# Kernel optimization log

Hardware: AMD Instinct MI355X
Metric: run time of the kernel (lower is better)

The kernel has to match this reference:

```python
import jax, jax.numpy as jnp
import numpy as np

B, N1, N2, D, L, H = 2, 384, 384, 128, 3, 128
DM_MIN = 0.5


def _gat_layer(x, adj, W, Wb, A, gW, gb):
    # GAT_gate from jaechanglim/DTI_PDBbind: attention softmax over dim 1, gated residual
    h = x @ W + Wb                                   # [B,N,D]
    e = jnp.einsum('bjl,bkl->bjk', h @ A, h)
    e = e + jnp.swapaxes(e, 1, 2)
    att = jnp.where(adj > 0, e, -9e15)
    att = jax.nn.softmax(att, axis=1) * adj
    h_prime = jax.nn.relu(jnp.einsum('bij,bjk->bik', att, h))
    coeff = jax.nn.sigmoid(jnp.concatenate([x, h_prime], -1) @ gW + gb)  # [B,N,1]
    return coeff * x + (1.0 - coeff) * h_prime


def _pair_mlp(h1g, h2g, W1, b1, W2, b2):
    # MLP(concat(h1_i, h2_j)) without materializing the [B,N1,N2,2D] concat:
    # split W1 into ligand / protein halves and broadcast-add the projections.
    p1 = jnp.einsum('bnd,dk->bnk', h1g, W1[:D])      # [B,N1,H]
    p2 = jnp.einsum('bmd,dk->bmk', h2g, W1[D:])      # [B,N2,H]
    hid = jax.nn.relu(p1[:, :, None, :] + p2[:, None, :, :] + b1)  # [B,N1,N2,H]
    return (hid @ W2 + b2)[..., 0]                   # [B,N1,N2]


def reference(h1, adj1, h2, dmv, charge1, charge2, vdw_epsilon, vdw_sigma,
              delta_uff, valid1, valid2, no_metal1, no_metal2,
              node_W, gat_W, gat_Wb, gat_A, gat_gW, gat_gb,
              pair_W1, pair_b1, pair_W2, pair_b2,
              vdw_coeff, duff_coeff, int_W1, int_b1, int_W2, int_b2):
    h1g = h1 @ node_W
    h2g = h2 @ node_W
    for i in range(L):  # only ligand graph is convolved (as in the source)
        h1g = _gat_layer(h1g, adj1, gat_W[i], gat_Wb[i], gat_A[i], gat_gW[i], gat_gb[i])

    dm = jnp.sqrt(jnp.sum(dmv * dmv, -1) + 1e-10)    # [B,N1,N2]
    dm = jnp.where(dm < DM_MIN, 1e10, dm)

    # coulomb term (pair MLPs 0,1)
    cA = jax.nn.sigmoid(_pair_mlp(h1g, h2g, pair_W1[0], pair_b1[0], pair_W2[0], pair_b2[0]))
    cN = jax.nn.sigmoid(_pair_mlp(h1g, h2g, pair_W1[1], pair_b1[1], pair_W2[1], pair_b2[1])) * 2.0 + 1.0
    charge12 = charge1[:, :, None] * charge2[:, None, :]
    e_c = cA * charge12 * jnp.power(1.0 / dm, cN)
    e_c = e_c * valid1[:, :, None] * valid2[:, None, :]
    e_c = jnp.clip(e_c, -100.0, 100.0)
    e_c = jnp.sum(e_c, axis=(1, 2))[:, None]

    # vdw term (pair MLPs 2=A sigmoid, 3=B tanh, 4=N sigmoid)
    vA = (jax.nn.sigmoid(_pair_mlp(h1g, h2g, pair_W1[2], pair_b1[2], pair_W2[2], pair_b2[2])) * 0.6 + 0.7)
    vA = vA * (vdw_coeff[0] * vdw_coeff[0]) * vdw_epsilon
    vB = jnp.tanh(_pair_mlp(h1g, h2g, pair_W1[3], pair_b1[3], pair_W2[3], pair_b2[3])) * 0.6 + 0.7
    vN = jax.nn.sigmoid(_pair_mlp(h1g, h2g, pair_W1[4], pair_b1[4], pair_W2[4], pair_b2[4])) * 2.0 + 5.0
    dm0 = vdw_sigma * vB
    dm0 = jnp.where(dm0 < 1e-4, 1.0, dm0)
    r = jnp.power(dm0 / dm, vN)
    e_v = vA * (r * r - 2.0 * r)                     # (dm0/dm)^(2N) - 2(dm0/dm)^N
    e_v = e_v * no_metal1[:, :, None] * no_metal2[:, None, :]
    e_v = jnp.minimum(e_v, 100.0)
    e_v = jnp.sum(e_v, axis=(1, 2))[:, None]

    # conformational energy difference term
    e_u = (duff_coeff[0] * duff_coeff[0] * delta_uff)[:, None]

    # learned intercept from pooled ligand features
    hs = jnp.sum(h1g * valid1[..., None], axis=1)
    inter = jax.nn.relu(hs @ int_W1 + int_b1) @ int_W2 + int_b2

    return jnp.concatenate([e_c, e_v, e_u, inter], -1)  # [B,4]


def setup_inputs() -> dict:
    key = jax.random.key(0)
    ks = jax.random.split(key, 24)
    inp = {}
    inp['h1'] = jax.random.normal(ks[0], (B, N1, 54), jnp.float32)
    inp['h2'] = jax.random.normal(ks[1], (B, N2, 54), jnp.float32)
    a = jax.random.uniform(ks[2], (B, N1, N1))
    adj = (a > 0.9).astype(jnp.float32)
    adj = jnp.maximum(adj, jnp.swapaxes(adj, 1, 2))
    inp['adj1'] = jnp.maximum(adj, jnp.eye(N1, dtype=jnp.float32)[None])
    inp['dmv'] = jax.random.normal(ks[3], (B, N1, N2, 3), jnp.float32) * 3.0
    inp['charge1'] = jax.random.normal(ks[4], (B, N1), jnp.float32) * 0.3
    inp['charge2'] = jax.random.normal(ks[5], (B, N2), jnp.float32) * 0.3
    inp['vdw_epsilon'] = jax.random.uniform(ks[6], (B, N1, N2), jnp.float32) * 0.3
    inp['vdw_sigma'] = 3.0 + jax.random.uniform(ks[7], (B, N1, N2), jnp.float32)
    inp['delta_uff'] = jax.random.uniform(ks[8], (B,), jnp.float32) * 5.0
    inp['valid1'] = jnp.ones((B, N1), jnp.float32)
    inp['valid2'] = jnp.ones((B, N2), jnp.float32)
    inp['no_metal1'] = jnp.ones((B, N1), jnp.float32)
    inp['no_metal2'] = jnp.ones((B, N2), jnp.float32)
    # parameters
    inp['node_W'] = jax.random.normal(ks[9], (54, D), jnp.float32) * 0.1
    inp['gat_W'] = jax.random.normal(ks[10], (L, D, D), jnp.float32) * (1.0 / np.sqrt(D))
    inp['gat_Wb'] = jnp.zeros((L, D), jnp.float32)
    inp['gat_A'] = jax.random.normal(ks[11], (L, D, D), jnp.float32) * 0.05
    inp['gat_gW'] = jax.random.normal(ks[12], (L, 2 * D, 1), jnp.float32) * 0.05
    inp['gat_gb'] = jnp.zeros((L, 1), jnp.float32)
    inp['pair_W1'] = jax.random.normal(ks[13], (5, 2 * D, H), jnp.float32) * 0.05
    inp['pair_b1'] = jnp.zeros((5, H), jnp.float32)
    inp['pair_W2'] = jax.random.normal(ks[14], (5, H, 1), jnp.float32) * 0.1
    inp['pair_b2'] = jnp.zeros((5, 1), jnp.float32)
    inp['vdw_coeff'] = jnp.array([0.02], jnp.float32)
    inp['duff_coeff'] = jnp.array([0.1], jnp.float32)
    inp['int_W1'] = jax.random.normal(ks[15], (D, H), jnp.float32) * 0.05
    inp['int_b1'] = jnp.zeros((H,), jnp.float32)
    inp['int_W2'] = jax.random.normal(ks[16], (H, 1), jnp.float32) * 0.1
    inp['int_b2'] = jnp.zeros((1,), jnp.float32)
    return inp
```

## Files before the change

### kernel.cpp

```cpp
#include <hip/hip_runtime.h>
#include <math.h>

#define NN 384
#define DD 128
#define HH 128

__device__ __forceinline__ float sigmoidf_(float x) { return 1.f / (1.f + __expf(-x)); }
__device__ __forceinline__ float tanhf_(float x)    { return 1.f - 2.f / (__expf(2.f * x) + 1.f); }

__global__ __launch_bounds__(256) void k_start(
    const float* __restrict__ h1, const float* __restrict__ h2,
    const float* __restrict__ nW,
    const float* __restrict__ W, const float* __restrict__ Wb, const float* __restrict__ A,
    const float* __restrict__ pW1,
    const float* __restrict__ delta_uff, const float* __restrict__ duff,
    float* __restrict__ h1g, float* __restrict__ h2g,
    float* __restrict__ hb, float* __restrict__ hAb,
    float* __restrict__ hT, float* __restrict__ hAT,
    float* __restrict__ p2q, float* __restrict__ out) {
  int blk = blockIdx.x, tid = threadIdx.x, c = tid & 127, g = tid >> 7;
  if (blk == 0 && tid < 8) {
    int bb = tid >> 2, cc = tid & 3;
    out[tid] = (cc == 2) ? duff[0] * duff[0] * delta_uff[bb] : 0.f;
  }
  if (blk < 384) {
    int r = blk * 2 + g;
    const float* xr = h1 + r * 54;
    float acc = 0.f;
#pragma unroll 6
    for (int k = 0; k < 54; ++k) acc += xr[k] * nW[k * DD + c];
    h1g[r * DD + c] = acc;
    __syncthreads();
    const float4* xr4 = (const float4*)(h1g + r * DD);
    float a0 = 0.f, a1 = 0.f;
#pragma unroll 4
    for (int k4 = 0; k4 < DD / 4; ++k4) {
      float4 xv = xr4[k4]; int k = 4 * k4;
      a0 += xv.x * W[k * DD + c] + xv.z * W[(k + 2) * DD + c];
      a1 += xv.y * W[(k + 1) * DD + c] + xv.w * W[(k + 3) * DD + c];
    }
    float hv = a0 + a1 + Wb[c];
    hb[r * DD + c] = hv; hT[c * 768 + r] = hv;
    __syncthreads();
    const float4* hr4 = (const float4*)(hb + r * DD);
    a0 = 0.f; a1 = 0.f;
#pragma unroll 4
    for (int k4 = 0; k4 < DD / 4; ++k4) {
      float4 xv = hr4[k4]; int k = 4 * k4;
      a0 += xv.x * A[k * DD + c] + xv.z * A[(k + 2) * DD + c];
      a1 += xv.y * A[(k + 1) * DD + c] + xv.w * A[(k + 3) * DD + c];
    }
    float av = a0 + a1;
    hAb[r * DD + c] = av; hAT[c * 768 + r] = av;
  } else {
    int r0 = (blk - 384) * 2;
    int r = r0 + g;
    const float* xr = h2 + r * 54;
    float acc = 0.f;
#pragma unroll 6
    for (int k = 0; k < 54; ++k) acc += xr[k] * nW[k * DD + c];
    h2g[r * DD + c] = acc;
    __syncthreads();
    const float* xbase = h2g + r0 * DD;
    for (int o = tid; o < 640; o += 256) {
      int m = o >> 7, hc = o & 127;
      const float* Wcol = pW1 + (m * 256 + 128) * HH + hc;
      float a0 = 0.f, a1 = 0.f;
#pragma unroll 4
      for (int k = 0; k < DD; ++k) {
        float w = Wcol[k * HH];
        a0 += xbase[k] * w;
        a1 += xbase[DD + k] * w;
      }
      float* dst = p2q + (size_t)((m * 32 + (hc >> 2)) * 768 + r0) * 4 + (hc & 3);
      dst[0] = a0; dst[4] = a1;
    }
  }
}

__global__ __launch_bounds__(384) void k_att(
    const float* __restrict__ hb, const float* __restrict__ hAb,
    const float* __restrict__ hT, const float* __restrict__ hAT,
    const float* __restrict__ adj, float* __restrict__ att) {
  int col = blockIdx.x;
  int b = col / NN, k = col - b * NN;
  int tid = threadIdx.x;
  const float* hrow  = hb  + col * DD;
  const float* harow = hAb + col * DD;
  const float* hTb   = hT  + b * NN + tid;
  const float* hATb  = hAT + b * NN + tid;
  float e0 = 0.f, e1 = 0.f;
#pragma unroll 4
  for (int cc = 0; cc < DD; cc += 2) {
    e0 += hATb[cc * 768] * hrow[cc] + hTb[cc * 768] * harow[cc];
    e1 += hATb[(cc + 1) * 768] * hrow[cc + 1] + hTb[(cc + 1) * 768] * harow[cc + 1];
  }
  float e = e0 + e1;
  float a = adj[col * NN + tid];
  __shared__ float red[6];
  float lmax = (a > 0.f) ? e : -3e38f;
#pragma unroll
  for (int off = 32; off > 0; off >>= 1) lmax = fmaxf(lmax, __shfl_down(lmax, off));
  int w = tid >> 6;
  if ((tid & 63) == 0) red[w] = lmax;
  __syncthreads();
  float m = red[0];
#pragma unroll
  for (int q = 1; q < 6; ++q) m = fmaxf(m, red[q]);
  float v = (a > 0.f) ? __expf(e - m) : 0.f;
  float s = v;
#pragma unroll
  for (int off = 32; off > 0; off >>= 1) s += __shfl_down(s, off);
  __syncthreads();
  if ((tid & 63) == 0) red[w] = s;
  __syncthreads();
  float d = 0.f;
#pragma unroll
  for (int q = 0; q < 6; ++q) d += red[q];
  att[(b * NN + tid) * NN + k] = v * a / d;
}

__global__ __launch_bounds__(256) void k_out_hhA(
    const float* __restrict__ x, const float* __restrict__ hb,
    const float* __restrict__ att,
    const float* __restrict__ gW, const float* __restrict__ gb,
    const float* __restrict__ Wn, const float* __restrict__ Wbn,
    const float* __restrict__ An,
    float* __restrict__ xout,
    float* __restrict__ hbn, float* __restrict__ hAbn,
    float* __restrict__ hTn, float* __restrict__ hATn) {
  int r = blockIdx.x;
  int b = r / NN;
  int tid = threadIdx.x, c = tid & 127, jh = tid >> 7;
  __shared__ float ph[2][DD];
  __shared__ float redw[2];
  const float4* ar4 = (const float4*)(att + r * NN) + jh * 48;
  const float* hp = hb + (b * NN + jh * 192) * DD + c;
  float q0 = 0.f, q1 = 0.f, q2 = 0.f, q3 = 0.f;
#pragma unroll 4
  for (int j4 = 0; j4 < 48; ++j4) {
    float4 av = ar4[j4];
    const float* hj = hp + j4 * 4 * DD;
    q0 += av.x * hj[0];
    q1 += av.y * hj[DD];
    q2 += av.z * hj[2 * DD];
    q3 += av.w * hj[3 * DD];
  }
  ph[jh][c] = (q0 + q1) + (q2 + q3);
  __syncthreads();
  float hpr = 0.f, xr = 0.f;
  if (tid < 128) {
    hpr = fmaxf(ph[0][c] + ph[1][c], 0.f);
    xr = x[r * DD + c];
    float v = xr * gW[c] + hpr * gW[DD + c];
#pragma unroll
    for (int off = 32; off > 0; off >>= 1) v += __shfl_down(v, off);
    if ((tid & 63) == 0) redw[tid >> 6] = v;
  }
  __syncthreads();
  if (tid < 128) {
    float coeff = sigmoidf_(redw[0] + redw[1] + gb[0]);
    xout[r * DD + c] = coeff * xr + (1.f - coeff) * hpr;
  }
  __syncthreads();
  const float* xb = xout + r * DD + jh * 64;
  const float* Wp = Wn + (jh * 64) * DD + c;
  float a0 = 0.f, a1 = 0.f;
#pragma unroll 4
  for (int k = 0; k < 64; k += 2) {
    a0 += xb[k] * Wp[k * DD];
    a1 += xb[k + 1] * Wp[(k + 1) * DD];
  }
  ph[jh][c] = a0 + a1;
  __syncthreads();
  if (tid < 128) {
    float hv = ph[0][c] + ph[1][c] + Wbn[c];
    hbn[r * DD + c] = hv; hTn[c * 768 + r] = hv;
  }
  __syncthreads();
  const float* hbr = hbn + r * DD + jh * 64;
  const float* Ap = An + (jh * 64) * DD + c;
  a0 = 0.f; a1 = 0.f;
#pragma unroll 4
  for (int k = 0; k < 64; k += 2) {
    a0 += hbr[k] * Ap[k * DD];
    a1 += hbr[k + 1] * Ap[(k + 1) * DD];
  }
  ph[jh][c] = a0 + a1;
  __syncthreads();
  if (tid < 128) {
    float av = ph[0][c] + ph[1][c];
    hAbn[r * DD + c] = av; hATn[c * 768 + r] = av;
  }
}

__global__ __launch_bounds__(256) void k_out_proj(
    const float* __restrict__ x, const float* __restrict__ hb,
    const float* __restrict__ att,
    const float* __restrict__ gW, const float* __restrict__ gb,
    const float* __restrict__ pW1, const float* __restrict__ pb1,
    const float* __restrict__ valid1,
    float* __restrict__ xout, float* __restrict__ p1, float* __restrict__ wsi) {
  int r = blockIdx.x;
  int b = r / NN;
  int tid = threadIdx.x, c = tid & 127, jh = tid >> 7;
  __shared__ float ph[2][DD];
  __shared__ float redw[2];
  const float4* ar4 = (const float4*)(att + r * NN) + jh * 48;
  const float* hp = hb + (b * NN + jh * 192) * DD + c;
  float q0 = 0.f, q1 = 0.f, q2 = 0.f, q3 = 0.f;
#pragma unroll 4
  for (int j4 = 0; j4 < 48; ++j4) {
    float4 av = ar4[j4];
    const float* hj = hp + j4 * 4 * DD;
    q0 += av.x * hj[0];
    q1 += av.y * hj[DD];
    q2 += av.z * hj[2 * DD];
    q3 += av.w * hj[3 * DD];
  }
  ph[jh][c] = (q0 + q1) + (q2 + q3);
  __syncthreads();
  float hpr = 0.f, xr = 0.f;
  if (tid < 128) {
    hpr = fmaxf(ph[0][c] + ph[1][c], 0.f);
    xr = x[r * DD + c];
    float v = xr * gW[c] + hpr * gW[DD + c];
#pragma unroll
    for (int off = 32; off > 0; off >>= 1) v += __shfl_down(v, off);
    if ((tid & 63) == 0) redw[tid >> 6] = v;
  }
  __syncthreads();
  if (tid < 128) {
    float coeff = sigmoidf_(redw[0] + redw[1] + gb[0]);
    float nv = coeff * xr + (1.f - coeff) * hpr;
    xout[r * DD + c] = nv;
    wsi[r * DD + c] = nv * valid1[r];
  }
  __syncthreads();
  const float* xbase = xout + r * DD;
  for (int o = tid; o < 640; o += 256) {
    int m = o >> 7, hc = o & 127;
    const float* Wcol = pW1 + (m * 256) * HH + hc;
    float a0 = 0.f, a1 = 0.f;
#pragma unroll 4
    for (int k = 0; k < DD; k += 2) {
      a0 += xbase[k] * Wcol[k * HH];
      a1 += xbase[k + 1] * Wcol[(k + 1) * HH];
    }
    p1[(r * 5 + m) * HH + hc] = a0 + a1 + pb1[m * HH + hc];
  }
}

__global__ __launch_bounds__(384) void k_energy(
    const float* __restrict__ p1, const float* __restrict__ p2q,
    const float* __restrict__ W2, const float* __restrict__ b2,
    const float* __restrict__ dmv, const float* __restrict__ charge1,
    const float* __restrict__ charge2, const float* __restrict__ veps,
    const float* __restrict__ vsig, const float* __restrict__ valid1,
    const float* __restrict__ valid2, const float* __restrict__ nm1,
    const float* __restrict__ nm2, const float* __restrict__ vdw_coeff,
    float* __restrict__ out) {
  int blk = blockIdx.x, tid = threadIdx.x;
  int tile = blk >> 1, jh = blk & 1;
  int r0 = tile * 3;
  int b = r0 / NN;
  int jp = tid < 192 ? tid : tid - 192;
  int hh = tid < 192 ? 0 : 1;
  int j = jh * 192 + jp;
  int col = b * NN + j;
  const float* q0 = p1 + (r0 + 0) * 640;
  const float* q1 = p1 + (r0 + 1) * 640;
  const float* q2 = p1 + (r0 + 2) * 640;
  const float4* p2q4 = (const float4*)p2q;
  float am[3][5];
#pragma unroll
  for (int m = 0; m < 5; ++m) {
    const float4* pc = p2q4 + (size_t)(m * 32 + hh * 16) * 768 + col;
    const float* w2m = W2 + m * HH + hh * 64;
    const float* x0 = q0 + m * HH + hh * 64;
    const float* x1 = q1 + m * HH + hh * 64;
    const float* x2 = q2 + m * HH + hh * 64;
    float a0 = 0.f, a1 = 0.f, a2 = 0.f;
#pragma unroll 4
    for (int hq = 0; hq < 16; ++hq) {
      float4 pv = pc[(size_t)hq * 768];
      float w0 = w2m[4 * hq], w1 = w2m[4 * hq + 1], w2v = w2m[4 * hq + 2], w3 = w2m[4 * hq + 3];
      a0 += fmaxf(x0[4 * hq] + pv.x, 0.f) * w0 + fmaxf(x0[4 * hq + 1] + pv.y, 0.f) * w1
          + fmaxf(x0[4 * hq + 2] + pv.z, 0.f) * w2v + fmaxf(x0[4 * hq + 3] + pv.w, 0.f) * w3;
      a1 += fmaxf(x1[4 * hq] + pv.x, 0.f) * w0 + fmaxf(x1[4 * hq + 1] + pv.y, 0.f) * w1
          + fmaxf(x1[4 * hq + 2] + pv.z, 0.f) * w2v + fmaxf(x1[4 * hq + 3] + pv.w, 0.f) * w3;
      a2 += fmaxf(x2[4 * hq] + pv.x, 0.f) * w0 + fmaxf(x2[4 * hq + 1] + pv.y, 0.f) * w1
          + fmaxf(x2[4 * hq + 2] + pv.z, 0.f) * w2v + fmaxf(x2[4 * hq + 3] + pv.w, 0.f) * w3;
    }
    am[0][m] = a0; am[1][m] = a1; am[2][m] = a2;
  }
  __shared__ float part[192][15];
  if (hh) {
#pragma unroll
    for (int t = 0; t < 3; ++t)
#pragma unroll
      for (int m = 0; m < 5; ++m) part[jp][t * 5 + m] = am[t][m];
  }
  __syncthreads();
  __shared__ float rec[3], rev[3];
  if (!hh) {
#pragma unroll
    for (int t = 0; t < 3; ++t)
#pragma unroll
      for (int m = 0; m < 5; ++m) am[t][m] += part[jp][t * 5 + m] + b2[m];
    float q2c = charge2[col], vv2 = valid2[col], n2 = nm2[col];
    float vc2 = vdw_coeff[0] * vdw_coeff[0];
    float ec_sum = 0.f, ev_sum = 0.f;
#pragma unroll
    for (int ti = 0; ti < 3; ++ti) {
      int gi = r0 + ti;
      int pidx = gi * NN + j;
      float dx = dmv[pidx * 3], dy = dmv[pidx * 3 + 1], dz = dmv[pidx * 3 + 2];
      float dm = sqrtf(dx * dx + dy * dy + dz * dz + 1e-10f);
      if (dm < 0.5f) dm = 1e10f;
      float cA = sigmoidf_(am[ti][0]);
      float cN = sigmoidf_(am[ti][1]) * 2.f + 1.f;
      float e_c = cA * charge1[gi] * q2c * __powf(1.f / dm, cN);
      e_c *= valid1[gi] * vv2;
      e_c = fminf(fmaxf(e_c, -100.f), 100.f);
      ec_sum += e_c;
      float vA = (sigmoidf_(am[ti][2]) * 0.6f + 0.7f) * vc2 * veps[pidx];
      float vB = tanhf_(am[ti][3]) * 0.6f + 0.7f;
      float vN = sigmoidf_(am[ti][4]) * 2.f + 5.f;
      float dm0 = vsig[pidx] * vB;
      if (dm0 < 1e-4f) dm0 = 1.f;
      float rr = __powf(dm0 / dm, vN);
      float e_v = vA * (rr * rr - 2.f * rr);
      e_v *= nm1[gi] * n2;
      e_v = fminf(e_v, 100.f);
      ev_sum += e_v;
    }
#pragma unroll
    for (int off = 32; off > 0; off >>= 1) {
      ec_sum += __shfl_down(ec_sum, off);
      ev_sum += __shfl_down(ev_sum, off);
    }
    if ((tid & 63) == 0) { rec[tid >> 6] = ec_sum; rev[tid >> 6] = ev_sum; }
  }
  __syncthreads();
  if (tid == 0) {
    atomicAdd(&out[b * 4 + 0], rec[0] + rec[1] + rec[2]);
    atomicAdd(&out[b * 4 + 1], rev[0] + rev[1] + rev[2]);
  }
}

__global__ __launch_bounds__(256) void k_fin(
    const float* __restrict__ wsi, const float* __restrict__ iW1,
    const float* __restrict__ ib1, const float* __restrict__ iW2,
    const float* __restrict__ ib2, float* __restrict__ out) {
  int tid = threadIdx.x, bb = tid >> 7, cc = tid & 127;
  __shared__ float hsf[2][DD];
  __shared__ float redf[2][2];
  float a0 = 0.f, a1 = 0.f;
  for (int q = 0; q < 384; q += 2) {
    a0 += wsi[(bb * 384 + q) * DD + cc];
    a1 += wsi[(bb * 384 + q + 1) * DD + cc];
  }
  hsf[bb][cc] = a0 + a1;
  __syncthreads();
  float hid = ib1[cc];
#pragma unroll 4
  for (int k = 0; k < DD; ++k) hid += hsf[bb][k] * iW1[k * HH + cc];
  hid = fmaxf(hid, 0.f);
  float v = hid * iW2[cc];
#pragma unroll
  for (int off = 32; off > 0; off >>= 1) v += __shfl_down(v, off);
  if ((tid & 63) == 0) redf[bb][(tid >> 6) & 1] = v;
  __syncthreads();
  if (tid < 2) out[tid * 4 + 3] = redf[tid][0] + redf[tid][1] + ib2[0];
}

extern "C" void kernel_launch(void* const* d_in, const int* in_sizes, int n_in,
                              void* d_out, int out_size, void* d_ws, size_t ws_size,
                              hipStream_t stream) {
  (void)in_sizes; (void)n_in; (void)out_size; (void)ws_size;
  const float* h1         = (const float*)d_in[0];
  const float* h2         = (const float*)d_in[1];
  const float* adj1       = (const float*)d_in[2];
  const float* dmv        = (const float*)d_in[3];
  const float* charge1    = (const float*)d_in[4];
  const float* charge2    = (const float*)d_in[5];
  const float* veps       = (const float*)d_in[6];
  const float* vsig       = (const float*)d_in[7];
  const float* delta_uff  = (const float*)d_in[8];
  const float* valid1     = (const float*)d_in[9];
  const float* valid2     = (const float*)d_in[10];
  const float* nm1        = (const float*)d_in[11];
  const float* nm2        = (const float*)d_in[12];
  const float* node_W     = (const float*)d_in[13];
  const float* gat_W      = (const float*)d_in[14];
  const float* gat_Wb     = (const float*)d_in[15];
  const float* gat_A      = (const float*)d_in[16];
  const float* gat_gW     = (const float*)d_in[17];
  const float* gat_gb     = (const float*)d_in[18];
  const float* pW1        = (const float*)d_in[19];
  const float* pb1        = (const float*)d_in[20];
  const float* pW2        = (const float*)d_in[21];
  const float* pb2        = (const float*)d_in[22];
  const float* vdw_coeff  = (const float*)d_in[23];
  const float* duff_coeff = (const float*)d_in[24];
  const float* iW1        = (const float*)d_in[25];
  const float* ib1        = (const float*)d_in[26];
  const float* iW2        = (const float*)d_in[27];
  const float* ib2        = (const float*)d_in[28];
  float* out = (float*)d_out;

  float* ws = (float*)d_ws;
  const int RN = 768 * DD;
  float* h1gA = ws;
  float* h1gB = h1gA + RN;
  float* h2g  = h1gB + RN;
  float* hb0  = h2g  + RN;
  float* hA0  = hb0  + RN;
  float* hT0  = hA0  + RN;
  float* hAT0 = hT0  + RN;
  float* hb1  = hAT0 + RN;
  float* hA1  = hb1  + RN;
  float* hT1  = hA1  + RN;
  float* hAT1 = hT1  + RN;
  float* att  = hAT1 + RN;
  float* p1   = att + 2 * NN * NN;
  float* p2q  = p1 + 768 * 640;
  float* wsi  = p2q + 768 * 640;

  const int DD2 = DD * DD;

  k_start<<<dim3(768), dim3(256), 0, stream>>>(
      h1, h2, node_W, gat_W, gat_Wb, gat_A, pW1, delta_uff, duff_coeff,
      h1gA, h2g, hb0, hA0, hT0, hAT0, p2q, out);

  k_att<<<dim3(768), dim3(384), 0, stream>>>(hb0, hA0, hT0, hAT0, adj1, att);
  k_out_hhA<<<dim3(768), dim3(256), 0, stream>>>(
      h1gA, hb0, att, gat_gW + 0, gat_gb + 0,
      gat_W + DD2, gat_Wb + DD, gat_A + DD2,
      h1gB, hb1, hA1, hT1, hAT1);
  k_att<<<dim3(768), dim3(384), 0, stream>>>(hb1, hA1, hT1, hAT1, adj1, att);
  k_out_hhA<<<dim3(768), dim3(256), 0, stream>>>(
      h1gB, hb1, att, gat_gW + 2 * DD, gat_gb + 1,
      gat_W + 2 * DD2, gat_Wb + 2 * DD, gat_A + 2 * DD2,
      h1gA, hb0, hA0, hT0, hAT0);
  k_att<<<dim3(768), dim3(384), 0, stream>>>(hb0, hA0, hT0, hAT0, adj1, att);
  k_out_proj<<<dim3(768), dim3(256), 0, stream>>>(
      h1gA, hb0, att, gat_gW + 4 * DD, gat_gb + 2,
      pW1, pb1, valid1, h1gB, p1, wsi);

  k_energy<<<dim3(512), dim3(384), 0, stream>>>(
      p1, p2q, pW2, pb2, dmv, charge1, charge2, veps, vsig,
      valid1, valid2, nm1, nm2, vdw_coeff, out);
  k_fin<<<dim3(1), dim3(256), 0, stream>>>(wsi, iW1, ib1, iW2, ib2, out);
}
```

Baseline: 326.4 us.

## Restructure pair-energy kernel per row pair and fold final MLP into it

The energy kernel changes decomposition. Each block now handles two ligand rows across all 384 protein columns, and each thread covers the full hidden dimension, so the shared-memory split-H reduction is gone. The separate single-block readout kernel becomes an extra block of the energy launch, saving one kernel launch. Loads of adjacency, gate weights, validity and distance inputs are hoisted ahead of the main loops so their latency overlaps compute. In exchange, p2q is re-read once per two rows instead of once per three, and the grid is smaller.

```diff
diff --git a/kernel.cpp b/kernel.cpp
--- a/kernel.cpp
+++ b/kernel.cpp
@@ -85,6 +85,7 @@
   int col = blockIdx.x;
   int b = col / NN, k = col - b * NN;
   int tid = threadIdx.x;
+  float a = adj[col * NN + tid];
   const float* hrow  = hb  + col * DD;
   const float* harow = hAb + col * DD;
   const float* hTb   = hT  + b * NN + tid;
@@ -96,7 +97,6 @@
     e1 += hATb[(cc + 1) * 768] * hrow[cc + 1] + hTb[(cc + 1) * 768] * harow[cc + 1];
   }
   float e = e0 + e1;
-  float a = adj[col * NN + tid];
   __shared__ float red[6];
   float lmax = (a > 0.f) ? e : -3e38f;
 #pragma unroll
@@ -134,6 +134,8 @@
   int tid = threadIdx.x, c = tid & 127, jh = tid >> 7;
   __shared__ float ph[2][DD];
   __shared__ float redw[2];
+  float xr = x[r * DD + c];
+  float g1 = gW[c], g2 = gW[DD + c], gbv = gb[0];
   const float4* ar4 = (const float4*)(att + r * NN) + jh * 48;
   const float* hp = hb + (b * NN + jh * 192) * DD + c;
   float q0 = 0.f, q1 = 0.f, q2 = 0.f, q3 = 0.f;
@@ -148,18 +150,17 @@
   }
   ph[jh][c] = (q0 + q1) + (q2 + q3);
   __syncthreads();
-  float hpr = 0.f, xr = 0.f;
+  float hpr = 0.f;
   if (tid < 128) {
     hpr = fmaxf(ph[0][c] + ph[1][c], 0.f);
-    xr = x[r * DD + c];
-    float v = xr * gW[c] + hpr * gW[DD + c];
+    float v = xr * g1 + hpr * g2;
 #pragma unroll
     for (int off = 32; off > 0; off >>= 1) v += __shfl_down(v, off);
     if ((tid & 63) == 0) redw[tid >> 6] = v;
   }
   __syncthreads();
   if (tid < 128) {
-    float coeff = sigmoidf_(redw[0] + redw[1] + gb[0]);
+    float coeff = sigmoidf_(redw[0] + redw[1] + gbv);
     xout[r * DD + c] = coeff * xr + (1.f - coeff) * hpr;
   }
   __syncthreads();
@@ -206,6 +207,9 @@
   int tid = threadIdx.x, c = tid & 127, jh = tid >> 7;
   __shared__ float ph[2][DD];
   __shared__ float redw[2];
+  float xr = x[r * DD + c];
+  float g1 = gW[c], g2 = gW[DD + c], gbv = gb[0];
+  float vld = valid1[r];
   const float4* ar4 = (const float4*)(att + r * NN) + jh * 48;
   const float* hp = hb + (b * NN + jh * 192) * DD + c;
   float q0 = 0.f, q1 = 0.f, q2 = 0.f, q3 = 0.f;
@@ -220,21 +224,20 @@
   }
   ph[jh][c] = (q0 + q1) + (q2 + q3);
   __syncthreads();
-  float hpr = 0.f, xr = 0.f;
+  float hpr = 0.f;
   if (tid < 128) {
     hpr = fmaxf(ph[0][c] + ph[1][c], 0.f);
-    xr = x[r * DD + c];
-    float v = xr * gW[c] + hpr * gW[DD + c];
+    float v = xr * g1 + hpr * g2;
 #pragma unroll
     for (int off = 32; off > 0; off >>= 1) v += __shfl_down(v, off);
     if ((tid & 63) == 0) redw[tid >> 6] = v;
   }
   __syncthreads();
   if (tid < 128) {
-    float coeff = sigmoidf_(redw[0] + redw[1] + gb[0]);
+    float coeff = sigmoidf_(redw[0] + redw[1] + gbv);
     float nv = coeff * xr + (1.f - coeff) * hpr;
     xout[r * DD + c] = nv;
-    wsi[r * DD + c] = nv * valid1[r];
+    wsi[r * DD + c] = nv * vld;
   }
   __syncthreads();
   const float* xbase = xout + r * DD;
@@ -259,120 +262,124 @@
     const float* __restrict__ vsig, const float* __restrict__ valid1,
     const float* __restrict__ valid2, const float* __restrict__ nm1,
     const float* __restrict__ nm2, const float* __restrict__ vdw_coeff,
-    float* __restrict__ out) {
-  int blk = blockIdx.x, tid = threadIdx.x;
-  int tile = blk >> 1, jh = blk & 1;
-  int r0 = tile * 3;
-  int b = r0 / NN;
-  int jp = tid < 192 ? tid : tid - 192;
-  int hh = tid < 192 ? 0 : 1;
-  int j = jh * 192 + jp;
-  int col = b * NN + j;
-  const float* q0 = p1 + (r0 + 0) * 640;
-  const float* q1 = p1 + (r0 + 1) * 640;
-  const float* q2 = p1 + (r0 + 2) * 640;
-  const float4* p2q4 = (const float4*)p2q;
-  float am[3][5];
-#pragma unroll
-  for (int m = 0; m < 5; ++m) {
-    const float4* pc = p2q4 + (size_t)(m * 32 + hh * 16) * 768 + col;
-    const float* w2m = W2 + m * HH + hh * 64;
-    const float* x0 = q0 + m * HH + hh * 64;
-    const float* x1 = q1 + m * HH + hh * 64;
-    const float* x2 = q2 + m * HH + hh * 64;
-    float a0 = 0.f, a1 = 0.f, a2 = 0.f;
-#pragma unroll 4
-    for (int hq = 0; hq < 16; ++hq) {
-      float4 pv = pc[(size_t)hq * 768];
-      float w0 = w2m[4 * hq], w1 = w2m[4 * hq + 1], w2v = w2m[4 * hq + 2], w3 = w2m[4 * hq + 3];
-      a0 += fmaxf(x0[4 * hq] + pv.x, 0.f) * w0 + fmaxf(x0[4 * hq + 1] + pv.y, 0.f) * w1
-          + fmaxf(x0[4 * hq + 2] + pv.z, 0.f) * w2v + fmaxf(x0[4 * hq + 3] + pv.w, 0.f) * w3;
-      a1 += fmaxf(x1[4 * hq] + pv.x, 0.f) * w0 + fmaxf(x1[4 * hq + 1] + pv.y, 0.f) * w1
-          + fmaxf(x1[4 * hq + 2] + pv.z, 0.f) * w2v + fmaxf(x1[4 * hq + 3] + pv.w, 0.f) * w3;
-      a2 += fmaxf(x2[4 * hq] + pv.x, 0.f) * w0 + fmaxf(x2[4 * hq + 1] + pv.y, 0.f) * w1
-          + fmaxf(x2[4 * hq + 2] + pv.z, 0.f) * w2v + fmaxf(x2[4 * hq + 3] + pv.w, 0.f) * w3;
-    }
-    am[0][m] = a0; am[1][m] = a1; am[2][m] = a2;
-  }
-  __shared__ float part[192][15];
-  if (hh) {
-#pragma unroll
-    for (int t = 0; t < 3; ++t)
-#pragma unroll
-      for (int m = 0; m < 5; ++m) part[jp][t * 5 + m] = am[t][m];
-  }
-  __syncthreads();
-  __shared__ float rec[3], rev[3];
-  if (!hh) {
-#pragma unroll
-    for (int t = 0; t < 3; ++t)
-#pragma unroll
-      for (int m = 0; m < 5; ++m) am[t][m] += part[jp][t * 5 + m] + b2[m];
-    float q2c = charge2[col], vv2 = valid2[col], n2 = nm2[col];
-    float vc2 = vdw_coeff[0] * vdw_coeff[0];
-    float ec_sum = 0.f, ev_sum = 0.f;
-#pragma unroll
-    for (int ti = 0; ti < 3; ++ti) {
-      int gi = r0 + ti;
-      int pidx = gi * NN + j;
-      float dx = dmv[pidx * 3], dy = dmv[pidx * 3 + 1], dz = dmv[pidx * 3 + 2];
-      float dm = sqrtf(dx * dx + dy * dy + dz * dz + 1e-10f);
-      if (dm < 0.5f) dm = 1e10f;
-      float cA = sigmoidf_(am[ti][0]);
-      float cN = sigmoidf_(am[ti][1]) * 2.f + 1.f;
-      float e_c = cA * charge1[gi] * q2c * __powf(1.f / dm, cN);
-      e_c *= valid1[gi] * vv2;
-      e_c = fminf(fmaxf(e_c, -100.f), 100.f);
-      ec_sum += e_c;
-      float vA = (sigmoidf_(am[ti][2]) * 0.6f + 0.7f) * vc2 * veps[pidx];
-      float vB = tanhf_(am[ti][3]) * 0.6f + 0.7f;
-      float vN = sigmoidf_(am[ti][4]) * 2.f + 5.f;
-      float dm0 = vsig[pidx] * vB;
-      if (dm0 < 1e-4f) dm0 = 1.f;
-      float rr = __powf(dm0 / dm, vN);
-      float e_v = vA * (rr * rr - 2.f * rr);
-      e_v *= nm1[gi] * n2;
-      e_v = fminf(e_v, 100.f);
-      ev_sum += e_v;
-    }
-#pragma unroll
-    for (int off = 32; off > 0; off >>= 1) {
-      ec_sum += __shfl_down(ec_sum, off);
-      ev_sum += __shfl_down(ev_sum, off);
-    }
-    if ((tid & 63) == 0) { rec[tid >> 6] = ec_sum; rev[tid >> 6] = ev_sum; }
-  }
-  __syncthreads();
-  if (tid == 0) {
-    atomicAdd(&out[b * 4 + 0], rec[0] + rec[1] + rec[2]);
-    atomicAdd(&out[b * 4 + 1], rev[0] + rev[1] + rev[2]);
-  }
-}
-
-__global__ __launch_bounds__(256) void k_fin(
     const float* __restrict__ wsi, const float* __restrict__ iW1,
     const float* __restrict__ ib1, const float* __restrict__ iW2,
     const float* __restrict__ ib2, float* __restrict__ out) {
-  int tid = threadIdx.x, bb = tid >> 7, cc = tid & 127;
-  __shared__ float hsf[2][DD];
-  __shared__ float redf[2][2];
-  float a0 = 0.f, a1 = 0.f;
-  for (int q = 0; q < 384; q += 2) {
-    a0 += wsi[(bb * 384 + q) * DD + cc];
-    a1 += wsi[(bb * 384 + q + 1) * DD + cc];
-  }
-  hsf[bb][cc] = a0 + a1;
-  __syncthreads();
-  float hid = ib1[cc];
-#pragma unroll 4
-  for (int k = 0; k < DD; ++k) hid += hsf[bb][k] * iW1[k * HH + cc];
-  hid = fmaxf(hid, 0.f);
-  float v = hid * iW2[cc];
-#pragma unroll
-  for (int off = 32; off > 0; off >>= 1) v += __shfl_down(v, off);
-  if ((tid & 63) == 0) redf[bb][(tid >> 6) & 1] = v;
-  __syncthreads();
-  if (tid < 2) out[tid * 4 + 3] = redf[tid][0] + redf[tid][1] + ib2[0];
+  int blk = blockIdx.x, tid = threadIdx.x;
+  if (blk >= 384) {
+    if (tid < 256) {
+      int bb = tid >> 7, cc = tid & 127;
+      __shared__ float hsf[2][DD];
+      __shared__ float redf[2][2];
+      float a0 = 0.f, a1 = 0.f;
+      for (int q = 0; q < 384; q += 2) {
+        a0 += wsi[(bb * 384 + q) * DD + cc];
+        a1 += wsi[(bb * 384 + q + 1) * DD + cc];
+      }
+      hsf[bb][cc] = a0 + a1;
+      __syncthreads();
+      float hid = ib1[cc];
+#pragma unroll 4
+      for (int k = 0; k < DD; ++k) hid += hsf[bb][k] * iW1[k * HH + cc];
+      hid = fmaxf(hid, 0.f);
+      float v = hid * iW2[cc];
+#pragma unroll
+      for (int off = 32; off > 0; off >>= 1) v += __shfl_down(v, off);
+      if ((tid & 63) == 0) redf[bb][(tid >> 6) & 1] = v;
+      __syncthreads();
+      if (tid < 2) out[tid * 4 + 3] = redf[tid][0] + redf[tid][1] + ib2[0];
+    }
+    return;
+  }
+  int r0 = blk * 2;
+  int b = r0 / NN;
+  int j = tid;
+  int col = b * NN + j;
+  int p0 = r0 * NN + j, pI = p0 + NN;
+  float dx0 = dmv[3 * p0], dy0 = dmv[3 * p0 + 1], dz0 = dmv[3 * p0 + 2];
+  float dx1 = dmv[3 * pI], dy1 = dmv[3 * pI + 1], dz1 = dmv[3 * pI + 2];
+  float ve0 = veps[p0], ve1 = veps[pI];
+  float vs0 = vsig[p0], vs1 = vsig[pI];
+  float q2c = charge2[col], vv2 = valid2[col], n2 = nm2[col];
+  float c1a = charge1[r0], c1b = charge1[r0 + 1];
+  float vaa = valid1[r0], vab = valid1[r0 + 1];
+  float naa = nm1[r0], nab = nm1[r0 + 1];
+  float vc2 = vdw_coeff[0] * vdw_coeff[0];
+
+  const float* q0 = p1 + (r0 + 0) * 640;
+  const float* q1 = p1 + (r0 + 1) * 640;
+  const float4* p2q4 = (const float4*)p2q;
+  float acc0[5], acc1[5];
+#pragma unroll
+  for (int m = 0; m < 5; ++m) {
+    const float4* pc = p2q4 + (size_t)(m * 32) * 768 + col;
+    const float* x0m = q0 + m * HH;
+    const float* x1m = q1 + m * HH;
+    const float* w2m = W2 + m * HH;
+    float a0 = 0.f, a1 = 0.f;
+#pragma unroll 8
+    for (int hq = 0; hq < 32; ++hq) {
+      float4 pv = pc[(size_t)hq * 768];
+      float w0 = w2m[4 * hq], w1 = w2m[4 * hq + 1];
+      float w2v = w2m[4 * hq + 2], w3 = w2m[4 * hq + 3];
+      a0 += fmaxf(x0m[4 * hq] + pv.x, 0.f) * w0 + fmaxf(x0m[4 * hq + 1] + pv.y, 0.f) * w1
+          + fmaxf(x0m[4 * hq + 2] + pv.z, 0.f) * w2v + fmaxf(x0m[4 * hq + 3] + pv.w, 0.f) * w3;
+      a1 += fmaxf(x1m[4 * hq] + pv.x, 0.f) * w0 + fmaxf(x1m[4 * hq + 1] + pv.y, 0.f) * w1
+          + fmaxf(x1m[4 * hq + 2] + pv.z, 0.f) * w2v + fmaxf(x1m[4 * hq + 3] + pv.w, 0.f) * w3;
+    }
+    acc0[m] = a0 + b2[m]; acc1[m] = a1 + b2[m];
+  }
+
+  float ec_sum = 0.f, ev_sum = 0.f;
+  {
+    float dm = sqrtf(dx0 * dx0 + dy0 * dy0 + dz0 * dz0 + 1e-10f);
+    if (dm < 0.5f) dm = 1e10f;
+    float cA = sigmoidf_(acc0[0]);
+    float cN = sigmoidf_(acc0[1]) * 2.f + 1.f;
+    float e_c = cA * c1a * q2c * __powf(1.f / dm, cN);
+    e_c *= vaa * vv2;
+    ec_sum += fminf(fmaxf(e_c, -100.f), 100.f);
+    float vA = (sigmoidf_(acc0[2]) * 0.6f + 0.7f) * vc2 * ve0;
+    float vB = tanhf_(acc0[3]) * 0.6f + 0.7f;
+    float vN = sigmoidf_(acc0[4]) * 2.f + 5.f;
+    float dm0 = vs0 * vB;
+    if (dm0 < 1e-4f) dm0 = 1.f;
+    float rr = __powf(dm0 / dm, vN);
+    float e_v = vA * (rr * rr - 2.f * rr) * naa * n2;
+    ev_sum += fminf(e_v, 100.f);
+  }
+  {
+    float dm = sqrtf(dx1 * dx1 + dy1 * dy1 + dz1 * dz1 + 1e-10f);
+    if (dm < 0.5f) dm = 1e10f;
+    float cA = sigmoidf_(acc1[0]);
+    float cN = sigmoidf_(acc1[1]) * 2.f + 1.f;
+    float e_c = cA * c1b * q2c * __powf(1.f / dm, cN);
+    e_c *= vab * vv2;
+    ec_sum += fminf(fmaxf(e_c, -100.f), 100.f);
+    float vA = (sigmoidf_(acc1[2]) * 0.6f + 0.7f) * vc2 * ve1;
+    float vB = tanhf_(acc1[3]) * 0.6f + 0.7f;
+    float vN = sigmoidf_(acc1[4]) * 2.f + 5.f;
+    float dm0 = vs1 * vB;
+    if (dm0 < 1e-4f) dm0 = 1.f;
+    float rr = __powf(dm0 / dm, vN);
+    float e_v = vA * (rr * rr - 2.f * rr) * nab * n2;
+    ev_sum += fminf(e_v, 100.f);
+  }
+#pragma unroll
+  for (int off = 32; off > 0; off >>= 1) {
+    ec_sum += __shfl_down(ec_sum, off);
+    ev_sum += __shfl_down(ev_sum, off);
+  }
+  __shared__ float rec[6], rev[6];
+  if ((tid & 63) == 0) { rec[tid >> 6] = ec_sum; rev[tid >> 6] = ev_sum; }
+  __syncthreads();
+  if (tid == 0) {
+    float a = 0.f, c = 0.f;
+#pragma unroll
+    for (int w = 0; w < 6; ++w) { a += rec[w]; c += rev[w]; }
+    atomicAdd(&out[b * 4 + 0], a);
+    atomicAdd(&out[b * 4 + 1], c);
+  }
 }
 
 extern "C" void kernel_launch(void* const* d_in, const int* in_sizes, int n_in,
@@ -449,8 +456,7 @@
       h1gA, hb0, att, gat_gW + 4 * DD, gat_gb + 2,
       pW1, pb1, valid1, h1gB, p1, wsi);
 
-  k_energy<<<dim3(512), dim3(384), 0, stream>>>(
+  k_energy<<<dim3(385), dim3(384), 0, stream>>>(
       p1, p2q, pW2, pb2, dmv, charge1, charge2, veps, vsig,
-      valid1, valid2, nm1, nm2, vdw_coeff, out);
-  k_fin<<<dim3(1), dim3(256), 0, stream>>>(wsi, iW1, ib1, iW2, ib2, out);
-}
+      valid1, valid2, nm1, nm2, vdw_coeff, wsi, iW1, ib1, iW2, ib2, out);
+}
```

Measured after the change: 294.1 us. -9.9%, faster.
